# Kernel optimization log

Hardware: AMD Instinct MI355X
Metric: run time of the kernel (lower is better)

The kernel has to match this reference:

```python
import jax, jax.numpy as jnp
import numpy as np

B, N, F, H = 2, 2048, 1024, 16
D = F // H  # head_dim = 64
SCALE = D ** -0.5


def setup_inputs() -> dict:
    key = jax.random.key(0)
    ks = jax.random.split(key, 5)
    std = F ** -0.5
    return {
        "x": jax.random.normal(ks[0], (B, N, F), dtype=jnp.float32),
        "Wq": jax.random.normal(ks[1], (F, F), dtype=jnp.float32) * std,
        "Wk": jax.random.normal(ks[2], (F, F), dtype=jnp.float32) * std,
        "Wv": jax.random.normal(ks[3], (F, F), dtype=jnp.float32) * std,
        "Wo": jax.random.normal(ks[4], (F, F), dtype=jnp.float32) * std,
        "bo": jnp.zeros((F,), dtype=jnp.float32),
    }


def reference(x, Wq, Wk, Wv, Wo, bo):
    b, n, f = x.shape
    # nn.Linear computes x @ W.T
    q = (x @ Wq.T).reshape(b, n, H, D).transpose(0, 2, 1, 3)  # bhnd
    k = (x @ Wk.T).reshape(b, n, H, D).transpose(0, 2, 1, 3)
    v = (x @ Wv.T).reshape(b, n, H, D).transpose(0, 2, 1, 3)
    score = jax.nn.softmax(jnp.einsum('bhif,bhjf->bhij', q, k) * SCALE, axis=-1)
    attn = jnp.einsum('bhij,bhjf->bihf', score, v)  # (b, n, h, d)
    o = attn.reshape(b, n, f) @ Wo.T + bo
    return o
```

## Files before the change

### kernel.cpp

```cpp
#include <hip/hip_runtime.h>
#include <hip/hip_bf16.h>

#define B_    2
#define NSEQ  2048
#define FDIM  1024
#define NH    16
#define HD    64
#define MTOT  (B_*NSEQ)
#define BHSZ  (NSEQ*HD)

typedef __bf16 bf16_t;
typedef __bf16 bf16x4 __attribute__((ext_vector_type(4)));
typedef __bf16 bf16x8 __attribute__((ext_vector_type(8)));
typedef float  f32x4  __attribute__((ext_vector_type(4)));

#define AS1 __attribute__((address_space(1)))
#define AS3 __attribute__((address_space(3)))

#if __has_builtin(__builtin_amdgcn_exp2f)
#define EXP2(x) __builtin_amdgcn_exp2f(x)
#else
#define EXP2(x) exp2f(x)
#endif

__device__ __forceinline__ void gld_lds16(const bf16_t* g, bf16_t* l) {
  __builtin_amdgcn_global_load_lds((const AS1 void*)g, (AS3 void*)l, 16, 0, 0);
}

extern "C" __global__ __launch_bounds__(256) void cast_all_k(
    const float* __restrict__ x,  const float* __restrict__ wq,
    const float* __restrict__ wk, const float* __restrict__ wv,
    const float* __restrict__ wo,
    bf16_t* __restrict__ xb,  bf16_t* __restrict__ wqb,
    bf16_t* __restrict__ wkb, bf16_t* __restrict__ wvb,
    bf16_t* __restrict__ wob)
{
  long t = (long)blockIdx.x * blockDim.x + threadIdx.x;
  long i = t * 4;
  const float* src; bf16_t* dst; long off;
  if      (i < 4194304L) { src = x;  dst = xb;  off = i; }
  else if (i < 5242880L) { src = wq; dst = wqb; off = i - 4194304L; }
  else if (i < 6291456L) { src = wk; dst = wkb; off = i - 5242880L; }
  else if (i < 7340032L) { src = wv; dst = wvb; off = i - 6291456L; }
  else                   { src = wo; dst = wob; off = i - 7340032L; }
  float4 v = *(const float4*)(src + off);
  bf16x4 o = { (bf16_t)v.x, (bf16_t)v.y, (bf16_t)v.z, (bf16_t)v.w };
  *(bf16x4*)(dst + off) = o;
}

extern "C" __global__ __launch_bounds__(512) void gemm_bt_k(
    const bf16_t* __restrict__ A,
    const bf16_t* __restrict__ Bq, const bf16_t* __restrict__ Bk,
    const bf16_t* __restrict__ Bv,
    bf16_t* __restrict__ oq, bf16_t* __restrict__ okk,
    bf16_t* __restrict__ ovt)
{
  __shared__ __align__(16) char garena[33792];
  bf16_t* As = (bf16_t*)garena;
  bf16_t* Bs = (bf16_t*)(garena + 16384);
  const int K = FDIM;
  int mode = blockIdx.z;
  const bf16_t* Bw = (mode == 0) ? Bq : (mode == 1) ? Bk : Bv;
  int m0 = blockIdx.x * 128, n0 = blockIdx.y * 128;
  int tid = threadIdx.x, lane = tid & 63, wave = tid >> 6;
  int g = lane >> 4, c = lane & 15;
  int wm = (wave & 1) * 64, wn = (wave >> 1) * 32;
  f32x4 acc[4][2];
  for (int i = 0; i < 4; ++i)
    for (int j = 0; j < 2; ++j)
      acc[i][j] = (f32x4){0.f, 0.f, 0.f, 0.f};

  int srow = lane >> 2;
  int scol = (lane & 3) * 8;

  for (int kt = 0; kt < K / 64; ++kt) {
    int kk = kt * 64;
    {
      int chunk = wave;
      const bf16_t* ag = A  + (long)(m0 + chunk*16 + srow) * K + kk + scol;
      const bf16_t* bg = Bw + (long)(n0 + chunk*16 + srow) * K + kk + scol;
      gld_lds16(ag,      As + chunk * 512);
      gld_lds16(ag + 32, As + 4096 + chunk * 512);
      gld_lds16(bg,      Bs + chunk * 512);
      gld_lds16(bg + 32, Bs + 4096 + chunk * 512);
    }
    __syncthreads();
    bf16x8 af[4][2], bfr[2][2];
    for (int t = 0; t < 4; ++t) {
      af[t][0]  = *(const bf16x8*)(As + (wm + t*16 + c) * 32 + g * 8);
      af[t][1]  = *(const bf16x8*)(As + 4096 + (wm + t*16 + c) * 32 + g * 8);
    }
    for (int t = 0; t < 2; ++t) {
      bfr[t][0] = *(const bf16x8*)(Bs + (wn + t*16 + c) * 32 + g * 8);
      bfr[t][1] = *(const bf16x8*)(Bs + 4096 + (wn + t*16 + c) * 32 + g * 8);
    }
    for (int mt = 0; mt < 4; ++mt)
      for (int nt = 0; nt < 2; ++nt) {
        acc[mt][nt] = __builtin_amdgcn_mfma_f32_16x16x32_bf16(
            af[mt][0], bfr[nt][0], acc[mt][nt], 0, 0, 0);
        acc[mt][nt] = __builtin_amdgcn_mfma_f32_16x16x32_bf16(
            af[mt][1], bfr[nt][1], acc[mt][nt], 0, 0, 0);
      }
    __syncthreads();
  }

  bf16_t* Tl = (bf16_t*)garena;
  float sc = (mode == 0) ? 0.18033688011112042f : 1.0f;
  if (mode < 2) {
    for (int mt = 0; mt < 4; ++mt)
      for (int nt = 0; nt < 2; ++nt) {
        int nloc = wn + nt*16 + c;
        for (int r = 0; r < 4; ++r) {
          int mloc = wm + mt*16 + g*4 + r;
          Tl[mloc*132 + nloc] = (bf16_t)(acc[mt][nt][r] * sc);
        }
      }
  } else {
    for (int mt = 0; mt < 4; ++mt)
      for (int nt = 0; nt < 2; ++nt) {
        int nloc = wn + nt*16 + c;
        int mloc = wm + mt*16 + g*4;
        bf16x4 pk = { (bf16_t)acc[mt][nt][0], (bf16_t)acc[mt][nt][1],
                      (bf16_t)acc[mt][nt][2], (bf16_t)acc[mt][nt][3] };
        *(bf16x4*)(Tl + nloc*132 + mloc) = pk;
      }
  }
  __syncthreads();

  int b = m0 >> 11, m0loc = m0 & 2047;
  int h0 = n0 >> 6, tile0 = m0loc >> 6;
  int hoff = (mode == 2) ? 16 : 4;
#pragma unroll
  for (int u = 0; u < 4; ++u) {
    int chunk = u * 512 + tid;
    bf16_t* dst;
    int sidx;
    if (mode == 0) {
      int headloc = chunk >> 10, o = chunk & 1023;
      int tokloc = o >> 3, dd = (o & 7) * 8;
      sidx = tokloc*132 + headloc*64 + dd;
      dst = oq + ((long)(b*NH + h0 + headloc) * NSEQ + m0loc) * HD + (long)o * 8;
    } else if (mode == 1) {
      int region = chunk >> 9, o = chunk & 511;
      int headloc = region >> 1, t = region & 1;
      int f = o >> 6, rest = o & 63;
      int mtA = f >> 1, kh = f & 1, gK = rest >> 4, cA = rest & 15;
      int tokloc = t*64 + mtA*16 + cA;
      sidx = tokloc*132 + headloc*64 + kh*32 + gK*8;
      dst = okk + (long)(b*NH + h0 + headloc) * BHSZ
            + (long)(tile0 + t) * 4096 + (long)o * 8;
    } else {
      int region = chunk >> 9, o = chunk & 511;
      int headloc = region >> 1, t = region & 1;
      int c2 = o >> 8, dt = (o >> 6) & 3, ln = o & 63;
      int gA = ln >> 4, cA = ln & 15;
      sidx = (headloc*64 + dt*16 + cA) * 132 + t*64 + c2*32 + gA*4;
      dst = ovt + (long)(b*NH + h0 + headloc) * BHSZ
            + (long)(tile0 + t) * 4096 + (long)o * 8;
    }
    bf16x4 lo = *(const bf16x4*)(Tl + sidx);
    bf16x4 hi = *(const bf16x4*)(Tl + sidx + hoff);
    bf16x8 v;
#pragma unroll
    for (int i = 0; i < 4; ++i) { v[i] = lo[i]; v[i+4] = hi[i]; }
    *(bf16x8*)dst = v;
  }
}

extern "C" __global__ __launch_bounds__(512) void gemm_out_k(
    const bf16_t* __restrict__ A, const bf16_t* __restrict__ W,
    const float* __restrict__ bias, float* __restrict__ out)
{
  __shared__ __align__(16) bf16_t As[8192];
  __shared__ __align__(16) bf16_t Bs[4096];
  const int K = FDIM;
  int m0 = blockIdx.x * 128, n0 = blockIdx.y * 64;
  int tid = threadIdx.x, lane = tid & 63, wave = tid >> 6;
  int g = lane >> 4, c = lane & 15;
  int wm = (wave & 3) * 32, wn = (wave >> 2) * 32;
  f32x4 acc[2][2];
  for (int i = 0; i < 2; ++i)
    for (int j = 0; j < 2; ++j)
      acc[i][j] = (f32x4){0.f, 0.f, 0.f, 0.f};

  int srow = lane >> 2;
  int scol = (lane & 3) * 8;

  for (int kt = 0; kt < K / 64; ++kt) {
    int kk = kt * 64;
    {
      const bf16_t* ag = A + (long)(m0 + wave*16 + srow) * K + kk + scol;
      gld_lds16(ag,      As + wave * 512);
      gld_lds16(ag + 32, As + 4096 + wave * 512);
      if (wave < 4) {
        const bf16_t* bg = W + (long)(n0 + wave*16 + srow) * K + kk + scol;
        gld_lds16(bg,      Bs + wave * 512);
        gld_lds16(bg + 32, Bs + 2048 + wave * 512);
      }
    }
    __syncthreads();
    bf16x8 af[2][2], bfr[2][2];
    for (int t = 0; t < 2; ++t) {
      af[t][0]  = *(const bf16x8*)(As + (wm + t*16 + c) * 32 + g * 8);
      af[t][1]  = *(const bf16x8*)(As + 4096 + (wm + t*16 + c) * 32 + g * 8);
      bfr[t][0] = *(const bf16x8*)(Bs + (wn + t*16 + c) * 32 + g * 8);
      bfr[t][1] = *(const bf16x8*)(Bs + 2048 + (wn + t*16 + c) * 32 + g * 8);
    }
    for (int mt = 0; mt < 2; ++mt)
      for (int nt = 0; nt < 2; ++nt) {
        acc[mt][nt] = __builtin_amdgcn_mfma_f32_16x16x32_bf16(
            af[mt][0], bfr[nt][0], acc[mt][nt], 0, 0, 0);
        acc[mt][nt] = __builtin_amdgcn_mfma_f32_16x16x32_bf16(
            af[mt][1], bfr[nt][1], acc[mt][nt], 0, 0, 0);
      }
    __syncthreads();
  }

  for (int mt = 0; mt < 2; ++mt)
    for (int nt = 0; nt < 2; ++nt) {
      int n = n0 + wn + nt*16 + c;
      float bv = bias[n];
      for (int r = 0; r < 4; ++r) {
        int m = m0 + wm + mt*16 + g*4 + r;
        out[(long)m * FDIM + n] = acc[mt][nt][r] + bv;
      }
    }
}

extern "C" __global__ __launch_bounds__(512) void attn_fused_k(
    const bf16_t* __restrict__ q, const bf16_t* __restrict__ k,
    const bf16_t* __restrict__ vt, bf16_t* __restrict__ attn)
{
  __shared__ __align__(16) char arena[65536];
  __shared__ float Ll[128];
  int bh = blockIdx.y;
  int tid = threadIdx.x, lane = tid & 63, wave = tid >> 6;
  int g = lane >> 4, c = lane & 15;
  int qg = wave & 3, half = wave >> 2;
  int qw = blockIdx.x * 128 + qg * 32;
  const bf16_t* Q  = q  + (long)bh * NSEQ * HD;
  const bf16_t* Kf = k  + (long)bh * BHSZ;
  const bf16_t* Vf = vt + (long)bh * BHSZ;

  bf16x8 bQ[2][2];
#pragma unroll
  for (int s = 0; s < 2; ++s)
#pragma unroll
    for (int hh = 0; hh < 2; ++hh)
      bQ[s][hh] = *(const bf16x8*)(Q + (long)(qw + s*16 + c) * HD + hh*32 + g*8);

  f32x4 acc[2][4];
  f32x4 lsum[2];
#pragma unroll
  for (int s = 0; s < 2; ++s) {
#pragma unroll
    for (int dt = 0; dt < 4; ++dt) acc[s][dt] = (f32x4){0.f, 0.f, 0.f, 0.f};
    lsum[s] = (f32x4){0.f, 0.f, 0.f, 0.f};
  }

  int w4 = wave & 3, ln = lane;
  const int NT = NSEQ / 128;
  int kbase = half * (NSEQ / 2);

  auto stage = [&](int buf, int k0) {
    bf16_t* Kb = (bf16_t*)(arena + buf * 32768 + half * 16384);
    bf16_t* Vb = Kb + 4096;
    long tbase = (long)(k0 >> 6) * 4096;
#pragma unroll
    for (int j = 0; j < 2; ++j) {
      int ch = j*4 + w4;
      gld_lds16(Kf + tbase + ch*512 + ln*8, Kb + ch*512);
      gld_lds16(Vf + tbase + ch*512 + ln*8, Vb + ch*512);
    }
  };

  stage(0, kbase);
  __syncthreads();

  for (int kt = 0; kt < NT; ++kt) {
    int cur = kt & 1;
    if (kt + 1 < NT) stage(cur ^ 1, kbase + (kt + 1) * 64);

    const bf16_t* Kb = (const bf16_t*)(arena + cur * 32768 + half * 16384);
    const bf16_t* Vb = Kb + 4096;

    f32x4 St[2][4];
#pragma unroll
    for (int mt = 0; mt < 4; ++mt) {
      bf16x8 k0f = *(const bf16x8*)(Kb + (mt*2 + 0) * 512 + lane * 8);
      bf16x8 k1f = *(const bf16x8*)(Kb + (mt*2 + 1) * 512 + lane * 8);
#pragma unroll
      for (int s = 0; s < 2; ++s) {
        f32x4 z = (f32x4){0.f, 0.f, 0.f, 0.f};
        z = __builtin_amdgcn_mfma_f32_16x16x32_bf16(k0f, bQ[s][0], z, 0, 0, 0);
        z = __builtin_amdgcn_mfma_f32_16x16x32_bf16(k1f, bQ[s][1], z, 0, 0, 0);
        St[s][mt] = z;
      }
    }

    bf16x8 bP[2][2];
#pragma unroll
    for (int s = 0; s < 2; ++s)
#pragma unroll
      for (int c2 = 0; c2 < 2; ++c2) {
        f32x4 pa = St[s][c2*2 + 0];
        f32x4 pb = St[s][c2*2 + 1];
        bf16x8 t;
#pragma unroll
        for (int r = 0; r < 4; ++r) {
          float x0 = EXP2(pa[r]);
          float x1 = EXP2(pb[r]);
          lsum[s][r] += x0 + x1;
          t[r]     = (bf16_t)x0;
          t[r + 4] = (bf16_t)x1;
        }
        bP[s][c2] = t;
      }

#pragma unroll
    for (int c2 = 0; c2 < 2; ++c2)
#pragma unroll
      for (int dt = 0; dt < 4; ++dt) {
        bf16x8 aV = *(const bf16x8*)(Vb + (c2*4 + dt) * 512 + lane * 8);
        acc[0][dt] = __builtin_amdgcn_mfma_f32_16x16x32_bf16(
            aV, bP[0][c2], acc[0][dt], 0, 0, 0);
        acc[1][dt] = __builtin_amdgcn_mfma_f32_16x16x32_bf16(
            aV, bP[1][c2], acc[1][dt], 0, 0, 0);
      }

    __syncthreads();
  }

  float lp[2];
#pragma unroll
  for (int s = 0; s < 2; ++s) {
    float p = (lsum[s][0] + lsum[s][1]) + (lsum[s][2] + lsum[s][3]);
    p += __shfl_xor(p, 16);
    p += __shfl_xor(p, 32);
    lp[s] = p;
  }

  float* Opart = (float*)arena;
  bf16_t* Tb = (bf16_t*)(arena + 36864);
  if (half == 1) {
#pragma unroll
    for (int s = 0; s < 2; ++s) {
      int qrow = qg*32 + s*16 + c;
#pragma unroll
      for (int dt = 0; dt < 4; ++dt)
        *(f32x4*)(Opart + qrow*72 + dt*16 + g*4) = acc[s][dt];
      if (g == 0) Ll[qrow] = lp[s];
    }
  }
  __syncthreads();
  if (half == 0) {
#pragma unroll
    for (int s = 0; s < 2; ++s) {
      int qrow = qg*32 + s*16 + c;
      float inv = 1.f / (lp[s] + Ll[qrow]);
#pragma unroll
      for (int dt = 0; dt < 4; ++dt) {
        f32x4 part = *(const f32x4*)(Opart + qrow*72 + dt*16 + g*4);
#pragma unroll
        for (int r = 0; r < 4; ++r)
          Tb[qrow*80 + dt*16 + g*4 + r] =
              (bf16_t)((acc[s][dt][r] + part[r]) * inv);
      }
    }
  }
  __syncthreads();
  int b = bh >> 4, h = bh & 15;
  int row = tid >> 2, dseg = (tid & 3) * 16;
  const bf16_t* src = Tb + row*80 + dseg;
  bf16_t* dst = attn + ((long)(b * NSEQ + blockIdx.x*128 + row)) * FDIM + h * HD + dseg;
  *(bf16x8*)(dst)     = *(const bf16x8*)(src);
  *(bf16x8*)(dst + 8) = *(const bf16x8*)(src + 8);
}

extern "C" void kernel_launch(void* const* d_in, const int* in_sizes, int n_in,
                              void* d_out, int out_size, void* d_ws, size_t ws_size,
                              hipStream_t stream)
{
  const float* x  = (const float*)d_in[0];
  const float* wq = (const float*)d_in[1];
  const float* wk = (const float*)d_in[2];
  const float* wv = (const float*)d_in[3];
  const float* wo = (const float*)d_in[4];
  const float* bo = (const float*)d_in[5];
  float* out = (float*)d_out;
  char* ws = (char*)d_ws;

  const size_t MB = 1024 * 1024;
  bf16_t* xb    = (bf16_t*)(ws);
  bf16_t* wqb   = (bf16_t*)(ws + 8  * MB);
  bf16_t* wkb   = (bf16_t*)(ws + 10 * MB);
  bf16_t* wvb   = (bf16_t*)(ws + 12 * MB);
  bf16_t* wob   = (bf16_t*)(ws + 14 * MB);
  bf16_t* q_ws  = (bf16_t*)(ws + 16 * MB);
  bf16_t* k_ws  = (bf16_t*)(ws + 24 * MB);
  bf16_t* vt_ws = (bf16_t*)(ws + 32 * MB);
  bf16_t* at_ws = (bf16_t*)(ws + 40 * MB);

  hipLaunchKernelGGL(cast_all_k, dim3(8192), dim3(256), 0, stream,
                     x, wq, wk, wv, wo, xb, wqb, wkb, wvb, wob);

  hipLaunchKernelGGL(gemm_bt_k, dim3(32, 8, 3), dim3(512), 0, stream,
                     xb, wqb, wkb, wvb, q_ws, k_ws, vt_ws);

  hipLaunchKernelGGL(attn_fused_k, dim3(16, 32), dim3(512), 0, stream,
                     q_ws, k_ws, vt_ws, at_ws);

  hipLaunchKernelGGL(gemm_out_k, dim3(32, 16), dim3(512), 0, stream,
                     at_ws, wob, bo, out);
}
```

Baseline: 174.5 us.

## Restructure attention blocks to 64 queries per block without key split

Each attention block now covers 64 queries with 4 waves of 16 queries each, and every wave walks the full key range. This removes the split-K halves and their cross-wave LDS reduction. The softmax row sum is computed with an MFMA against a ones vector instead of VALU adds plus shuffles, and s_setprio is raised around the MFMA sections. The grid doubles and LDS per block halves, which should raise occupancy. The cost is that K/V tiles are now loaded by more blocks and each wave does less work per tile load.

```diff
diff --git a/kernel.cpp b/kernel.cpp
--- a/kernel.cpp
+++ b/kernel.cpp
@@ -227,152 +227,113 @@
     }
 }
 
-extern "C" __global__ __launch_bounds__(512) void attn_fused_k(
+extern "C" __global__ __launch_bounds__(256) void attn_fused_k(
     const bf16_t* __restrict__ q, const bf16_t* __restrict__ k,
     const bf16_t* __restrict__ vt, bf16_t* __restrict__ attn)
 {
-  __shared__ __align__(16) char arena[65536];
-  __shared__ float Ll[128];
+  __shared__ __align__(16) char arena[32768];
   int bh = blockIdx.y;
   int tid = threadIdx.x, lane = tid & 63, wave = tid >> 6;
   int g = lane >> 4, c = lane & 15;
-  int qg = wave & 3, half = wave >> 2;
-  int qw = blockIdx.x * 128 + qg * 32;
+  int qw = blockIdx.x * 64 + wave * 16;
   const bf16_t* Q  = q  + (long)bh * NSEQ * HD;
   const bf16_t* Kf = k  + (long)bh * BHSZ;
   const bf16_t* Vf = vt + (long)bh * BHSZ;
 
-  bf16x8 bQ[2][2];
-#pragma unroll
-  for (int s = 0; s < 2; ++s)
-#pragma unroll
-    for (int hh = 0; hh < 2; ++hh)
-      bQ[s][hh] = *(const bf16x8*)(Q + (long)(qw + s*16 + c) * HD + hh*32 + g*8);
-
-  f32x4 acc[2][4];
-  f32x4 lsum[2];
-#pragma unroll
-  for (int s = 0; s < 2; ++s) {
-#pragma unroll
-    for (int dt = 0; dt < 4; ++dt) acc[s][dt] = (f32x4){0.f, 0.f, 0.f, 0.f};
-    lsum[s] = (f32x4){0.f, 0.f, 0.f, 0.f};
-  }
-
-  int w4 = wave & 3, ln = lane;
-  const int NT = NSEQ / 128;
-  int kbase = half * (NSEQ / 2);
-
-  auto stage = [&](int buf, int k0) {
-    bf16_t* Kb = (bf16_t*)(arena + buf * 32768 + half * 16384);
+  bf16x8 bQ[2];
+#pragma unroll
+  for (int hh = 0; hh < 2; ++hh)
+    bQ[hh] = *(const bf16x8*)(Q + (long)(qw + c) * HD + hh*32 + g*8);
+
+  f32x4 acc[4];
+#pragma unroll
+  for (int dt = 0; dt < 4; ++dt) acc[dt] = (f32x4){0.f, 0.f, 0.f, 0.f};
+  f32x4 accl = (f32x4){0.f, 0.f, 0.f, 0.f};
+
+  bf16x8 ones;
+#pragma unroll
+  for (int i = 0; i < 8; ++i) ones[i] = (bf16_t)1.0f;
+
+  const int NT = NSEQ / 64;
+
+  auto stage = [&](int buf, int t) {
+    bf16_t* Kb = (bf16_t*)(arena + buf * 16384);
     bf16_t* Vb = Kb + 4096;
-    long tbase = (long)(k0 >> 6) * 4096;
+    long tbase = (long)t * 4096;
 #pragma unroll
     for (int j = 0; j < 2; ++j) {
-      int ch = j*4 + w4;
-      gld_lds16(Kf + tbase + ch*512 + ln*8, Kb + ch*512);
-      gld_lds16(Vf + tbase + ch*512 + ln*8, Vb + ch*512);
+      int ch = j*4 + wave;
+      gld_lds16(Kf + tbase + ch*512 + lane*8, Kb + ch*512);
+      gld_lds16(Vf + tbase + ch*512 + lane*8, Vb + ch*512);
     }
   };
 
-  stage(0, kbase);
+  stage(0, 0);
   __syncthreads();
 
   for (int kt = 0; kt < NT; ++kt) {
     int cur = kt & 1;
-    if (kt + 1 < NT) stage(cur ^ 1, kbase + (kt + 1) * 64);
-
-    const bf16_t* Kb = (const bf16_t*)(arena + cur * 32768 + half * 16384);
+    if (kt + 1 < NT) stage(cur ^ 1, kt + 1);
+
+    const bf16_t* Kb = (const bf16_t*)(arena + cur * 16384);
     const bf16_t* Vb = Kb + 4096;
 
-    f32x4 St[2][4];
+    f32x4 St[4];
+    __builtin_amdgcn_s_setprio(1);
 #pragma unroll
     for (int mt = 0; mt < 4; ++mt) {
       bf16x8 k0f = *(const bf16x8*)(Kb + (mt*2 + 0) * 512 + lane * 8);
       bf16x8 k1f = *(const bf16x8*)(Kb + (mt*2 + 1) * 512 + lane * 8);
-#pragma unroll
-      for (int s = 0; s < 2; ++s) {
-        f32x4 z = (f32x4){0.f, 0.f, 0.f, 0.f};
-        z = __builtin_amdgcn_mfma_f32_16x16x32_bf16(k0f, bQ[s][0], z, 0, 0, 0);
-        z = __builtin_amdgcn_mfma_f32_16x16x32_bf16(k1f, bQ[s][1], z, 0, 0, 0);
-        St[s][mt] = z;
-      }
-    }
-
-    bf16x8 bP[2][2];
-#pragma unroll
-    for (int s = 0; s < 2; ++s)
-#pragma unroll
-      for (int c2 = 0; c2 < 2; ++c2) {
-        f32x4 pa = St[s][c2*2 + 0];
-        f32x4 pb = St[s][c2*2 + 1];
-        bf16x8 t;
-#pragma unroll
-        for (int r = 0; r < 4; ++r) {
-          float x0 = EXP2(pa[r]);
-          float x1 = EXP2(pb[r]);
-          lsum[s][r] += x0 + x1;
-          t[r]     = (bf16_t)x0;
-          t[r + 4] = (bf16_t)x1;
-        }
-        bP[s][c2] = t;
-      }
-
+      f32x4 z = (f32x4){0.f, 0.f, 0.f, 0.f};
+      z = __builtin_amdgcn_mfma_f32_16x16x32_bf16(k0f, bQ[0], z, 0, 0, 0);
+      z = __builtin_amdgcn_mfma_f32_16x16x32_bf16(k1f, bQ[1], z, 0, 0, 0);
+      St[mt] = z;
+    }
+    __builtin_amdgcn_s_setprio(0);
+
+    bf16x8 bP[2];
+#pragma unroll
+    for (int c2 = 0; c2 < 2; ++c2) {
+      f32x4 pa = St[c2*2 + 0];
+      f32x4 pb = St[c2*2 + 1];
+      bf16x8 t;
+#pragma unroll
+      for (int r = 0; r < 4; ++r) {
+        t[r]     = (bf16_t)EXP2(pa[r]);
+        t[r + 4] = (bf16_t)EXP2(pb[r]);
+      }
+      bP[c2] = t;
+    }
+
+    __builtin_amdgcn_s_setprio(1);
+    accl = __builtin_amdgcn_mfma_f32_16x16x32_bf16(ones, bP[0], accl, 0, 0, 0);
+    accl = __builtin_amdgcn_mfma_f32_16x16x32_bf16(ones, bP[1], accl, 0, 0, 0);
 #pragma unroll
     for (int c2 = 0; c2 < 2; ++c2)
 #pragma unroll
       for (int dt = 0; dt < 4; ++dt) {
         bf16x8 aV = *(const bf16x8*)(Vb + (c2*4 + dt) * 512 + lane * 8);
-        acc[0][dt] = __builtin_amdgcn_mfma_f32_16x16x32_bf16(
-            aV, bP[0][c2], acc[0][dt], 0, 0, 0);
-        acc[1][dt] = __builtin_amdgcn_mfma_f32_16x16x32_bf16(
-            aV, bP[1][c2], acc[1][dt], 0, 0, 0);
-      }
-
-    __syncthreads();
-  }
-
-  float lp[2];
-#pragma unroll
-  for (int s = 0; s < 2; ++s) {
-    float p = (lsum[s][0] + lsum[s][1]) + (lsum[s][2] + lsum[s][3]);
-    p += __shfl_xor(p, 16);
-    p += __shfl_xor(p, 32);
-    lp[s] = p;
-  }
-
-  float* Opart = (float*)arena;
-  bf16_t* Tb = (bf16_t*)(arena + 36864);
-  if (half == 1) {
-#pragma unroll
-    for (int s = 0; s < 2; ++s) {
-      int qrow = qg*32 + s*16 + c;
-#pragma unroll
-      for (int dt = 0; dt < 4; ++dt)
-        *(f32x4*)(Opart + qrow*72 + dt*16 + g*4) = acc[s][dt];
-      if (g == 0) Ll[qrow] = lp[s];
-    }
-  }
-  __syncthreads();
-  if (half == 0) {
-#pragma unroll
-    for (int s = 0; s < 2; ++s) {
-      int qrow = qg*32 + s*16 + c;
-      float inv = 1.f / (lp[s] + Ll[qrow]);
-#pragma unroll
-      for (int dt = 0; dt < 4; ++dt) {
-        f32x4 part = *(const f32x4*)(Opart + qrow*72 + dt*16 + g*4);
-#pragma unroll
-        for (int r = 0; r < 4; ++r)
-          Tb[qrow*80 + dt*16 + g*4 + r] =
-              (bf16_t)((acc[s][dt][r] + part[r]) * inv);
-      }
-    }
+        acc[dt] = __builtin_amdgcn_mfma_f32_16x16x32_bf16(
+            aV, bP[c2], acc[dt], 0, 0, 0);
+      }
+    __builtin_amdgcn_s_setprio(0);
+
+    __syncthreads();
+  }
+
+  float inv = 1.0f / accl[0];
+  bf16_t* Tb = (bf16_t*)arena;
+#pragma unroll
+  for (int dt = 0; dt < 4; ++dt) {
+    bf16x4 o = { (bf16_t)(acc[dt][0] * inv), (bf16_t)(acc[dt][1] * inv),
+                 (bf16_t)(acc[dt][2] * inv), (bf16_t)(acc[dt][3] * inv) };
+    *(bf16x4*)(Tb + (wave*16 + c)*80 + dt*16 + g*4) = o;
   }
   __syncthreads();
   int b = bh >> 4, h = bh & 15;
   int row = tid >> 2, dseg = (tid & 3) * 16;
   const bf16_t* src = Tb + row*80 + dseg;
-  bf16_t* dst = attn + ((long)(b * NSEQ + blockIdx.x*128 + row)) * FDIM + h * HD + dseg;
+  bf16_t* dst = attn + ((long)(b * NSEQ + blockIdx.x*64 + row)) * FDIM + h * HD + dseg;
   *(bf16x8*)(dst)     = *(const bf16x8*)(src);
   *(bf16x8*)(dst + 8) = *(const bf16x8*)(src + 8);
 }
@@ -407,7 +368,7 @@
   hipLaunchKernelGGL(gemm_bt_k, dim3(32, 8, 3), dim3(512), 0, stream,
                      xb, wqb, wkb, wvb, q_ws, k_ws, vt_ws);
 
-  hipLaunchKernelGGL(attn_fused_k, dim3(16, 32), dim3(512), 0, stream,
+  hipLaunchKernelGGL(attn_fused_k, dim3(32, 32), dim3(256), 0, stream,
                      q_ws, k_ws, vt_ws, at_ws);
 
   hipLaunchKernelGGL(gemm_out_k, dim3(32, 16), dim3(512), 0, stream,
```

After: 178.2 us. 2.1% more time.

## Software-pipeline QK, exp and PV across tiles with split K/V staging

Applied to the files above, without the earlier changes.

Restructures the attention inner loop into a two-stage software pipeline: the QK MFMAs for the next key tile are issued while the PV MFMAs for the current tile run, with exp/pack interleaved between PV halves. K and V are staged into separate double-buffered LDS slots so each can be loaded as late as needed. The softmax row sum is now computed with an extra MFMA against a ones vector instead of VALU adds and cross-lane shuffles, and s_setprio is raised around MFMA bursts. This aims to hide exp latency and memory waits behind matrix work, at the cost of more live registers and a more complex loop with more barriers. The sum is now taken over the bf16-rounded probabilities rather than the fp32 values.

```diff
diff --git a/kernel.cpp b/kernel.cpp
--- a/kernel.cpp
+++ b/kernel.cpp
@@ -250,41 +250,47 @@
       bQ[s][hh] = *(const bf16x8*)(Q + (long)(qw + s*16 + c) * HD + hh*32 + g*8);
 
   f32x4 acc[2][4];
-  f32x4 lsum[2];
+  f32x4 accl[2];
 #pragma unroll
   for (int s = 0; s < 2; ++s) {
 #pragma unroll
     for (int dt = 0; dt < 4; ++dt) acc[s][dt] = (f32x4){0.f, 0.f, 0.f, 0.f};
-    lsum[s] = (f32x4){0.f, 0.f, 0.f, 0.f};
-  }
+    accl[s] = (f32x4){0.f, 0.f, 0.f, 0.f};
+  }
+
+  bf16x8 ones;
+#pragma unroll
+  for (int i = 0; i < 8; ++i) ones[i] = (bf16_t)1.0f;
 
   int w4 = wave & 3, ln = lane;
   const int NT = NSEQ / 128;
-  int kbase = half * (NSEQ / 2);
-
-  auto stage = [&](int buf, int k0) {
-    bf16_t* Kb = (bf16_t*)(arena + buf * 32768 + half * 16384);
-    bf16_t* Vb = Kb + 4096;
-    long tbase = (long)(k0 >> 6) * 4096;
+  char* hbase = arena + half * 32768;
+
+  auto stageK = [&](int slot, int t) {
+    bf16_t* Kb = (bf16_t*)(hbase + slot * 8192);
+    long tbase = (long)(half * NT + t) * 4096;
 #pragma unroll
     for (int j = 0; j < 2; ++j) {
       int ch = j*4 + w4;
       gld_lds16(Kf + tbase + ch*512 + ln*8, Kb + ch*512);
+    }
+  };
+  auto stageV = [&](int slot, int t) {
+    bf16_t* Vb = (bf16_t*)(hbase + 16384 + slot * 8192);
+    long tbase = (long)(half * NT + t) * 4096;
+#pragma unroll
+    for (int j = 0; j < 2; ++j) {
+      int ch = j*4 + w4;
       gld_lds16(Vf + tbase + ch*512 + ln*8, Vb + ch*512);
     }
   };
 
-  stage(0, kbase);
-  __syncthreads();
-
-  for (int kt = 0; kt < NT; ++kt) {
-    int cur = kt & 1;
-    if (kt + 1 < NT) stage(cur ^ 1, kbase + (kt + 1) * 64);
-
-    const bf16_t* Kb = (const bf16_t*)(arena + cur * 32768 + half * 16384);
-    const bf16_t* Vb = Kb + 4096;
-
-    f32x4 St[2][4];
+  f32x4 St[2][4];
+  bf16x8 bPA[2][2], bPB[2][2];
+
+  auto qk = [&](int slot) {
+    const bf16_t* Kb = (const bf16_t*)(hbase + slot * 8192);
+    __builtin_amdgcn_s_setprio(1);
 #pragma unroll
     for (int mt = 0; mt < 4; ++mt) {
       bf16x8 k0f = *(const bf16x8*)(Kb + (mt*2 + 0) * 512 + lane * 8);
@@ -297,48 +303,70 @@
         St[s][mt] = z;
       }
     }
-
-    bf16x8 bP[2][2];
-#pragma unroll
-    for (int s = 0; s < 2; ++s)
-#pragma unroll
-      for (int c2 = 0; c2 < 2; ++c2) {
-        f32x4 pa = St[s][c2*2 + 0];
-        f32x4 pb = St[s][c2*2 + 1];
-        bf16x8 t;
-#pragma unroll
-        for (int r = 0; r < 4; ++r) {
-          float x0 = EXP2(pa[r]);
-          float x1 = EXP2(pb[r]);
-          lsum[s][r] += x0 + x1;
-          t[r]     = (bf16_t)x0;
-          t[r + 4] = (bf16_t)x1;
-        }
-        bP[s][c2] = t;
-      }
-
-#pragma unroll
-    for (int c2 = 0; c2 < 2; ++c2)
-#pragma unroll
-      for (int dt = 0; dt < 4; ++dt) {
-        bf16x8 aV = *(const bf16x8*)(Vb + (c2*4 + dt) * 512 + lane * 8);
-        acc[0][dt] = __builtin_amdgcn_mfma_f32_16x16x32_bf16(
-            aV, bP[0][c2], acc[0][dt], 0, 0, 0);
-        acc[1][dt] = __builtin_amdgcn_mfma_f32_16x16x32_bf16(
-            aV, bP[1][c2], acc[1][dt], 0, 0, 0);
-      }
-
+    __builtin_amdgcn_s_setprio(0);
+  };
+
+  auto expPack = [&](bf16x8 (&bP)[2][2], int c2) {
+#pragma unroll
+    for (int s = 0; s < 2; ++s) {
+      f32x4 pa = St[s][c2*2 + 0];
+      f32x4 pb = St[s][c2*2 + 1];
+      bf16x8 t;
+#pragma unroll
+      for (int r = 0; r < 4; ++r) {
+        t[r]     = (bf16_t)EXP2(pa[r]);
+        t[r + 4] = (bf16_t)EXP2(pb[r]);
+      }
+      bP[s][c2] = t;
+    }
+  };
+
+  auto pvPart = [&](int slot, bf16x8 (&bP)[2][2], int c2) {
+    const bf16_t* Vb = (const bf16_t*)(hbase + 16384 + slot * 8192);
+    __builtin_amdgcn_s_setprio(1);
+    accl[0] = __builtin_amdgcn_mfma_f32_16x16x32_bf16(ones, bP[0][c2], accl[0], 0, 0, 0);
+    accl[1] = __builtin_amdgcn_mfma_f32_16x16x32_bf16(ones, bP[1][c2], accl[1], 0, 0, 0);
+#pragma unroll
+    for (int dt = 0; dt < 4; ++dt) {
+      bf16x8 aV = *(const bf16x8*)(Vb + (c2*4 + dt) * 512 + lane * 8);
+      acc[0][dt] = __builtin_amdgcn_mfma_f32_16x16x32_bf16(
+          aV, bP[0][c2], acc[0][dt], 0, 0, 0);
+      acc[1][dt] = __builtin_amdgcn_mfma_f32_16x16x32_bf16(
+          aV, bP[1][c2], acc[1][dt], 0, 0, 0);
+    }
+    __builtin_amdgcn_s_setprio(0);
+  };
+
+  stageK(0, 0); stageV(0, 0); stageK(1, 1);
+  __syncthreads();
+  qk(0);
+  expPack(bPA, 0); expPack(bPA, 1);
+  __syncthreads();
+
+  for (int i = 0; i < NT / 2; ++i) {
+    int t0 = 2*i, t1 = t0 + 1;
+    if (t0 + 2 < NT) stageK(0, t0 + 2);
+    stageV(1, t0 + 1);
+    qk(1);
+    pvPart(0, bPA, 0);
+    expPack(bPB, 0);
+    pvPart(0, bPA, 1);
+    expPack(bPB, 1);
+    __syncthreads();
+    bool more = (t1 + 1 < NT);
+    if (t1 + 2 < NT) stageK(1, t1 + 2);
+    if (more) stageV(0, t1 + 1);
+    if (more) qk(0);
+    pvPart(1, bPB, 0);
+    if (more) expPack(bPA, 0);
+    pvPart(1, bPB, 1);
+    if (more) expPack(bPA, 1);
     __syncthreads();
   }
 
   float lp[2];
 #pragma unroll
-  for (int s = 0; s < 2; ++s) {
-    float p = (lsum[s][0] + lsum[s][1]) + (lsum[s][2] + lsum[s][3]);
-    p += __shfl_xor(p, 16);
-    p += __shfl_xor(p, 32);
-    lp[s] = p;
-  }
+  for (int s = 0; s < 2; ++s) lp[s] = accl[s][0];
 
   float* Opart = (float*)arena;
   bf16_t* Tb = (bf16_t*)(arena + 36864);
```

Result: no change. 177.2 us (+1.5%).
